# Optimization experiments

Hardware: AMD Instinct MI355X
Metric: run time of the kernel (lower is better)

## Reference

```python
import jax, jax.numpy as jnp
import numpy as np

B, NP, NC, E, C = 4, 512, 256, 128, 32
NBUCKET = 20


def soft_one_hot_linspace(x, start=0.0, end=15.0, number=NBUCKET):
    # e3nn soft_one_hot_linspace, basis='smooth_finite', cutoff=True
    values = jnp.linspace(start, end, number + 2)[1:-1]
    step = (end - start) / (number + 1)
    diff = (x[..., None] - values) / step

    def sus(y):  # exp(-1/y) for y>0 else 0 (smooth unit step)
        return jnp.where(y > 0.0, jnp.exp(-1.0 / jnp.where(y > 0.0, y, 1.0)), 0.0)

    return 1.14136 * jnp.exp(2.0) * sus(diff + 1.0) * sus(1.0 - diff)


def _init_linear(k, fan_in, fan_out):
    k1, k2 = jax.random.split(k)
    bound = 1.0 / np.sqrt(fan_in)
    W = jax.random.uniform(k1, (fan_in, fan_out), jnp.float32, -bound, bound)
    b = jax.random.uniform(k2, (fan_out,), jnp.float32, -bound, bound)
    return W, b


def setup_inputs() -> dict:
    key = jax.random.key(0)
    ks = jax.random.split(key, 12)
    inp = {}
    inp["z"] = jax.random.normal(ks[0], (B, NP, NC, E), jnp.float32)
    inp["z_mask"] = jax.random.randint(ks[1], (B, NP, NC), 0, 2) == 1
    inp["pocket_rep"] = jax.random.normal(ks[2], (B, NP, E), jnp.float32)
    inp["candidate_dis"] = jax.random.uniform(ks[3], (B, NP, NC), jnp.float32) * 16.0
    inp["W_lin"], inp["b_lin"] = _init_linear(ks[4], E, C)
    inp["W_dis"], inp["b_dis"] = _init_linear(ks[5], NBUCKET, C)
    inp["W_energy"], inp["b_energy"] = _init_linear(ks[6], C, 1)
    inp["W_gate"], inp["b_gate"] = _init_linear(ks[7], C, 1)
    inp["bias"] = jnp.ones((1,), jnp.float32)
    inp["W_energy_p"], inp["b_energy_p"] = _init_linear(ks[8], C, 1)
    inp["W_gate_p"], inp["b_gate_p"] = _init_linear(ks[9], C, 1)
    inp["bias_p"] = jnp.ones((1,), jnp.float32)
    inp["W_out"], inp["b_out"] = _init_linear(ks[10], E * C, E)
    return inp


def reference(z, z_mask, pocket_rep, candidate_dis,
              W_lin, b_lin, W_dis, b_dis,
              W_energy, b_energy, W_gate, b_gate, bias,
              W_energy_p, b_energy_p, W_gate_p, b_gate_p, bias_p,
              W_out, b_out):
    b, n_p, n_c, e = z.shape
    c = W_lin.shape[1]
    # linear + transpose(3,1): [B,Np,Nc,E] -> [B,C,Nc,Np]
    zc = jnp.transpose(z @ W_lin + b_lin, (0, 3, 2, 1))
    # softmax over last dim (Np)
    zc = jax.nn.softmax(zc, axis=-1)
    # distance-bucket bias: [B,Np,Nc,20] -> [B,Np,Nc,C] -> view [B,C,Nc,Np]
    edge_emb = soft_one_hot_linspace(candidate_dis)
    dis_bias = (edge_emb @ W_dis + b_dis).reshape(b, c, n_c, n_p)
    zc = zc + dis_bias
    # z_mask.repeat(C,1,1).view(B,C,Nc,Np) -- literal torch element order
    mask_rep = jnp.tile(z_mask, (c, 1, 1)).reshape(b, c, n_c, n_p)
    zc = jnp.where(mask_rep, jnp.asarray(1e-09, zc.dtype), zc)
    # gated energy heads on z.transpose(3,1): [B,Np,Nc,C]
    zt = jnp.transpose(zc, (0, 3, 2, 1))
    zm = z_mask.astype(zc.dtype)
    pair_energy = (jax.nn.sigmoid(zt @ W_gate + b_gate) * (zt @ W_energy + b_energy))[..., 0] * zm
    affinity_pred = jax.nn.leaky_relu(bias + pair_energy.sum(axis=(-1, -2)))
    pair_energy_p = (jax.nn.sigmoid(zt @ W_gate_p + b_gate_p) * (zt @ W_energy_p + b_energy_p))[..., 0] * zm
    prmsd_pred = jax.nn.leaky_relu(bias_p + pair_energy_p.sum(axis=(-1, -2)))
    # ligand rep: bmm([B,C*Nc,Np], [B,Np,E]) -> [B,Nc,C*E] -> Linear
    lig = jnp.einsum('bcln,bne->bcle', zc, pocket_rep)  # [B,C,Nc,E]
    lig = jnp.transpose(lig, (0, 2, 1, 3)).reshape(b, n_c, c * e)
    ligand_rep = lig @ W_out + b_out
    return (ligand_rep, affinity_pred, prmsd_pred)
```

## Files before the change

kernel.cpp:

```cpp
#include <hip/hip_runtime.h>
#include <stdint.h>


typedef float f32x4 __attribute__((ext_vector_type(4)));
typedef short s16x8 __attribute__((ext_vector_type(8)));

#define DEV static __device__ __forceinline__

DEV unsigned short f2bf(float f) {
  unsigned u = __builtin_bit_cast(unsigned, f);
  u += 0x7FFFu + ((u >> 16) & 1u);
  return (unsigned short)(u >> 16);
}
DEV float bf2f(unsigned short h) {
  unsigned u = ((unsigned)h) << 16;
  return __builtin_bit_cast(float, u);
}

__global__ void prep_k(const float* __restrict__ wlin,
                       const float* __restrict__ pocket,
                       const int* __restrict__ zmask,
                       const float* __restrict__ cdis,
                       unsigned short* __restrict__ wtlin,
                       unsigned short* __restrict__ pt,
                       unsigned long long* __restrict__ zmb,
                       unsigned long long* __restrict__ smb,
                       float* __restrict__ cdisT,
                       float* __restrict__ accg) {
  for (int i = blockIdx.x * 256 + threadIdx.x; i < 1839112; i += gridDim.x * 256) {
    if (i < 524288) {
      int np = i & 511, nc = (i >> 9) & 255, b = i >> 17;
      unsigned long long bal = __ballot(zmask[b * 131072 + np * 256 + nc] != 0);
      if ((i & 63) == 0) zmb[i >> 6] = bal;
    } else if (i < 1048576) {
      int o = i - 524288;
      int nn = o & 511, cm = (o >> 9) & 3, nc = o >> 11;
      unsigned long long bal = __ballot(zmask[cm * 131072 + nc * 512 + nn] != 0);
      if ((o & 63) == 0) smb[o >> 6] = bal;
    } else if (i < 1310720) {
      int o = i - 1048576;
      int np = o & 511, e = (o >> 9) & 127, b = o >> 16;
      pt[o] = f2bf(pocket[(b * 512 + np) * 128 + e]);
    } else if (i < 1314816) {
      int o = i - 1310720;
      int k = o & 127, c = o >> 7;
      wtlin[o] = f2bf(wlin[k * 32 + c]);
    } else if (i < 1314824) {
      accg[i - 1314816] = 0.0f;
    } else {
      int o = i - 1314824;
      int c = o & 31, np5 = (o >> 5) & 15, nc = (o >> 9) & 255, b = o >> 17;
      cdisT[o] = cdis[(b * 512 + 16 * c + (nc >> 4)) * 256 + 16 * (nc & 15) + np5];
    }
  }
}

__global__ void tr_k(const float* __restrict__ wout,
                     unsigned short* __restrict__ wto) {
  __shared__ float tile[64][65];
  const int kt = blockIdx.x, et = blockIdx.y;
  const int t = threadIdx.x;
  const int col = t & 63, r0 = t >> 6;
#pragma unroll
  for (int rr = 0; rr < 16; ++rr) {
    int row = rr * 4 + r0;
    tile[row][col] = wout[(kt * 64 + row) * 128 + et * 64 + col];
  }
  __syncthreads();
#pragma unroll
  for (int rr = 0; rr < 16; ++rr) {
    int erow = rr * 4 + r0;
    wto[(et * 64 + erow) * 4096 + kt * 64 + col] = f2bf(tile[col][erow]);
  }
}

extern __shared__ char smem[];

__global__ __launch_bounds__(256, 3) void mega_k(
    const float* __restrict__ z,
    const float* __restrict__ cdisT,
    const float* __restrict__ wdis, const float* __restrict__ bdis_g,
    const float* __restrict__ wE, const float* __restrict__ bE,
    const float* __restrict__ wG, const float* __restrict__ bG,
    const float* __restrict__ wEp, const float* __restrict__ bEp,
    const float* __restrict__ wGp, const float* __restrict__ bGp,
    const unsigned short* __restrict__ wtlin,
    const unsigned short* __restrict__ pt,
    const unsigned long long* __restrict__ zmb,
    const unsigned long long* __restrict__ smb,
    unsigned short* __restrict__ lig, float* __restrict__ accg) {
  const int nc = blockIdx.x, b = blockIdx.y;
  const int t = threadIdx.x;
  const int w = t >> 6, ln = t & 63;
  const int m16 = ln & 15, q = ln >> 4;

  unsigned short* T = (unsigned short*)smem;

  __shared__ float s_wd[640];
  __shared__ float s_bd[32];
  __shared__ float s_we[32], s_wg[32], s_wep[32], s_wgp[32];
  __shared__ float s_red[160];
  __shared__ float s_gmax[32], s_gsum[32];
  __shared__ unsigned long long s_mb[4][8];
  __shared__ unsigned long long s_zw[8];
  __shared__ float s_r8[8];

  if (t < 32) {
    s_bd[t] = bdis_g[t];
    s_we[t] = wE[t]; s_wg[t] = wG[t];
    s_wep[t] = wEp[t]; s_wgp[t] = wGp[t];
    s_mb[t >> 3][t & 7] = smb[nc * 32 + t];
  }
  if (t >= 32 && t < 40) s_zw[t - 32] = zmb[(b * 256 + nc) * 8 + (t - 32)];
  for (int i = t; i < 640; i += 256) s_wd[i] = wdis[i];

  f32x4 acc1[8][2];
#pragma unroll
  for (int i = 0; i < 8; ++i) {
    acc1[i][0] = f32x4{0.f, 0.f, 0.f, 0.f};
    acc1[i][1] = f32x4{0.f, 0.f, 0.f, 0.f};
  }
  const float* zb = z + (size_t)b * 16777216 + (size_t)nc * 128;
  for (int k0 = 0; k0 < 128; k0 += 32) {
    s16x8 bf0 = *(const s16x8*)(wtlin + m16 * 128 + k0 + q * 8);
    s16x8 bf1 = *(const s16x8*)(wtlin + (16 + m16) * 128 + k0 + q * 8);
#pragma unroll
    for (int bt = 0; bt < 4; ++bt) {
      f32x4 z0[2], z1[2];
#pragma unroll
      for (int i = 0; i < 2; ++i) {
        int np = (w * 8 + bt * 2 + i) * 16 + m16;
        const float* p = zb + (size_t)np * 32768 + k0 + q * 8;
        z0[i] = *(const f32x4*)p;
        z1[i] = *(const f32x4*)(p + 4);
      }
#pragma unroll
      for (int i = 0; i < 2; ++i) {
        s16x8 af;
        af[0] = (short)f2bf(z0[i][0]); af[1] = (short)f2bf(z0[i][1]);
        af[2] = (short)f2bf(z0[i][2]); af[3] = (short)f2bf(z0[i][3]);
        af[4] = (short)f2bf(z1[i][0]); af[5] = (short)f2bf(z1[i][1]);
        af[6] = (short)f2bf(z1[i][2]); af[7] = (short)f2bf(z1[i][3]);
        int ai = bt * 2 + i;
        acc1[ai][0] = __builtin_amdgcn_mfma_f32_16x16x32_bf16(af, bf0, acc1[ai][0], 0, 0, 0);
        acc1[ai][1] = __builtin_amdgcn_mfma_f32_16x16x32_bf16(af, bf1, acc1[ai][1], 0, 0, 0);
      }
    }
  }

  float mx[2] = {-3.0e38f, -3.0e38f};
#pragma unroll
  for (int ai = 0; ai < 8; ++ai)
#pragma unroll
    for (int ct = 0; ct < 2; ++ct)
#pragma unroll
      for (int r = 0; r < 4; ++r) mx[ct] = fmaxf(mx[ct], acc1[ai][ct][r]);
#pragma unroll
  for (int ct = 0; ct < 2; ++ct) {
    float v = mx[ct];
    v = fmaxf(v, __shfl_xor(v, 16));
    v = fmaxf(v, __shfl_xor(v, 32));
    mx[ct] = v;
  }
  if (ln < 16) { s_red[ln * 5 + w] = mx[0]; s_red[(16 + ln) * 5 + w] = mx[1]; }
  __syncthreads();
  if (t < 32)
    s_gmax[t] = fmaxf(fmaxf(s_red[t * 5], s_red[t * 5 + 1]),
                      fmaxf(s_red[t * 5 + 2], s_red[t * 5 + 3]));
  __syncthreads();
  float sm[2] = {0.f, 0.f};
#pragma unroll
  for (int ct = 0; ct < 2; ++ct) {
    float g = s_gmax[ct * 16 + m16];
#pragma unroll
    for (int ai = 0; ai < 8; ++ai)
#pragma unroll
      for (int r = 0; r < 4; ++r) {
        float e = __expf(acc1[ai][ct][r] - g);
        acc1[ai][ct][r] = e;
        sm[ct] += e;
      }
  }
#pragma unroll
  for (int ct = 0; ct < 2; ++ct) {
    float v = sm[ct];
    v += __shfl_xor(v, 16);
    v += __shfl_xor(v, 32);
    sm[ct] = v;
  }
  if (ln < 16) { s_red[ln * 5 + w] = sm[0]; s_red[(16 + ln) * 5 + w] = sm[1]; }
  __syncthreads();
  if (t < 32)
    s_gsum[t] = 1.0f / (s_red[t * 5] + s_red[t * 5 + 1] + s_red[t * 5 + 2] + s_red[t * 5 + 3]);
  __syncthreads();

#pragma unroll
  for (int ct = 0; ct < 2; ++ct) {
    int c = ct * 16 + m16;
    float s = s_gsum[c];
#pragma unroll
    for (int ai = 0; ai < 8; ++ai) {
      int npb = (w * 8 + ai) * 16 + q * 4;
      unsigned lo = (unsigned)f2bf(acc1[ai][ct][0] * s) |
                    ((unsigned)f2bf(acc1[ai][ct][1] * s) << 16);
      unsigned hi = (unsigned)f2bf(acc1[ai][ct][2] * s) |
                    ((unsigned)f2bf(acc1[ai][ct][3] * s) << 16);
      *(uint2*)(T + c * 520 + npb) = make_uint2(lo, hi);
    }
  }
  __syncthreads();

  {
    const float SUSK = 8.4335794f;
    const float* cdb = cdisT + (size_t)(b * 256 + nc) * 512;
#pragma unroll
    for (int tt = 0; tt < 2; ++tt) {
      int task = t + tt * 256;
      int c = task & 31, np5 = task >> 5;
      float d = cdb[task];
      float val[32];
#pragma unroll
      for (int kk = 0; kk < 32; ++kk) val[kk] = s_bd[kk];
      for (int j = 0; j < 20; ++j) {
        float diff = d * (21.0f / 15.0f) - (float)(j + 1);
        float y1 = diff + 1.f, y2 = 1.f - diff;
        float u = 0.f;
        if (y1 > 0.f && y2 > 0.f) u = SUSK * __expf(-1.f / y1 - 1.f / y2);
#pragma unroll
        for (int kk = 0; kk < 32; ++kk) val[kk] += u * s_wd[j * 32 + kk];
      }
      int npb = np5 * 32;
      unsigned long long mw = s_mb[c & 3][npb >> 6];
#pragma unroll
      for (int kb2 = 0; kb2 < 4; ++kb2) {
        unsigned short* tp = T + c * 520 + npb + kb2 * 8;
        s16x8 tv = *(s16x8*)tp;
        s16x8 ov;
#pragma unroll
        for (int kk = 0; kk < 8; ++kk) {
          float x = bf2f((unsigned short)tv[kk]) + val[kb2 * 8 + kk];
          int mk = (int)((mw >> ((npb + kb2 * 8 + kk) & 63)) & 1ull);
          ov[kk] = (short)f2bf(mk ? 1e-9f : x);
        }
        *(s16x8*)tp = ov;
      }
    }
  }
  __syncthreads();

  {
    float aff = 0.f, prm = 0.f;
    const float bg0 = bG[0], be0 = bE[0], bgp0 = bGp[0], bep0 = bEp[0];
#pragma unroll
    for (int s = 0; s < 2; ++s) {
      int np = s * 256 + t;
      float g = bg0, e = be0, gp = bgp0, ep = bep0;
      for (int c = 0; c < 32; ++c) {
        float tv = bf2f(T[c * 520 + np]);
        g += tv * s_wg[c]; e += tv * s_we[c];
        gp += tv * s_wgp[c]; ep += tv * s_wep[c];
      }
      if ((s_zw[np >> 6] >> (np & 63)) & 1ull) {
        aff += e / (1.f + __expf(-g));
        prm += ep / (1.f + __expf(-gp));
      }
    }
#pragma unroll
    for (int d = 32; d >= 1; d >>= 1) {
      aff += __shfl_xor(aff, d);
      prm += __shfl_xor(prm, d);
    }
    if (ln == 0) { s_r8[w] = aff; s_r8[4 + w] = prm; }
    __syncthreads();
    if (t == 0) {
      atomicAdd(accg + b, s_r8[0] + s_r8[1] + s_r8[2] + s_r8[3]);
      atomicAdd(accg + 4 + b, s_r8[4] + s_r8[5] + s_r8[6] + s_r8[7]);
    }
  }

  {
    f32x4 a5[2][2];
    a5[0][0] = f32x4{0.f, 0.f, 0.f, 0.f}; a5[0][1] = a5[0][0];
    a5[1][0] = a5[0][0]; a5[1][1] = a5[0][0];
    const unsigned short* ptb = pt + b * 65536;
    for (int k0 = 0; k0 < 512; k0 += 32) {
      s16x8 aT0 = *(const s16x8*)(T + m16 * 520 + k0 + q * 8);
      s16x8 aT1 = *(const s16x8*)(T + (16 + m16) * 520 + k0 + q * 8);
      s16x8 bP0 = *(const s16x8*)(ptb + (w * 32 + m16) * 512 + k0 + q * 8);
      s16x8 bP1 = *(const s16x8*)(ptb + (w * 32 + 16 + m16) * 512 + k0 + q * 8);
      a5[0][0] = __builtin_amdgcn_mfma_f32_16x16x32_bf16(aT0, bP0, a5[0][0], 0, 0, 0);
      a5[0][1] = __builtin_amdgcn_mfma_f32_16x16x32_bf16(aT0, bP1, a5[0][1], 0, 0, 0);
      a5[1][0] = __builtin_amdgcn_mfma_f32_16x16x32_bf16(aT1, bP0, a5[1][0], 0, 0, 0);
      a5[1][1] = __builtin_amdgcn_mfma_f32_16x16x32_bf16(aT1, bP1, a5[1][1], 0, 0, 0);
    }
    unsigned short* lg = lig + (size_t)(b * 256 + nc) * 4096;
#pragma unroll
    for (int mt = 0; mt < 2; ++mt)
#pragma unroll
      for (int u = 0; u < 2; ++u)
#pragma unroll
        for (int r = 0; r < 4; ++r) {
          int c = mt * 16 + q * 4 + r;
          int e = w * 32 + u * 16 + m16;
          lg[c * 128 + e] = f2bf(a5[mt][u][r]);
        }
  }
}

__global__ __launch_bounds__(256, 2) void proj_k(
    const unsigned short* __restrict__ lig, const unsigned short* __restrict__ wto,
    float* __restrict__ part) {
  const int mb = blockIdx.x, ks = blockIdx.y;
  const int t = threadIdx.x, w = t >> 6, ln = t & 63;
  const int m16 = ln & 15, q = ln >> 4;
  f32x4 acc[8];
#pragma unroll
  for (int nt = 0; nt < 8; ++nt) acc[nt] = f32x4{0.f, 0.f, 0.f, 0.f};
  const int kb = ks * 512;
  const int row = mb * 64 + w * 16 + m16;
  for (int k0 = 0; k0 < 512; k0 += 32) {
    s16x8 af = *(const s16x8*)(lig + (size_t)row * 4096 + kb + k0 + q * 8);
    s16x8 bf[8];
#pragma unroll
    for (int nt = 0; nt < 8; ++nt)
      bf[nt] = *(const s16x8*)(wto + (size_t)(nt * 16 + m16) * 4096 + kb + k0 + q * 8);
#pragma unroll
    for (int nt = 0; nt < 8; ++nt)
      acc[nt] = __builtin_amdgcn_mfma_f32_16x16x32_bf16(af, bf[nt], acc[nt], 0, 0, 0);
  }
  float* pp = part + (size_t)ks * 131072 + (size_t)(mb * 64 + w * 16) * 128;
#pragma unroll
  for (int nt = 0; nt < 8; ++nt)
#pragma unroll
    for (int r = 0; r < 4; ++r)
      pp[(q * 4 + r) * 128 + nt * 16 + m16] = acc[nt][r];
}

__global__ void reduce_k(const float* __restrict__ part, const float* __restrict__ bout,
                         const float* __restrict__ accg, const float* __restrict__ bias,
                         const float* __restrict__ biasp, float* __restrict__ outp) {
  int i = blockIdx.x * 256 + threadIdx.x;
  float s = bout[i & 127];
#pragma unroll
  for (int ks = 0; ks < 8; ++ks) s += part[(size_t)ks * 131072 + i];
  outp[i] = s;
  if (blockIdx.x == 0 && threadIdx.x < 8) {
    int tt = threadIdx.x;
    float base = (tt < 4) ? bias[0] : biasp[0];
    float x = base + accg[tt];
    outp[131072 + tt] = (x >= 0.f) ? x : 0.01f * x;
  }
}

extern "C" void kernel_launch(void* const* d_in, const int* in_sizes, int n_in,
                              void* d_out, int out_size, void* d_ws, size_t ws_size,
                              hipStream_t stream) {
  const float* z      = (const float*)d_in[0];
  const int*   zmask  = (const int*)d_in[1];
  const float* pocket = (const float*)d_in[2];
  const float* cdis   = (const float*)d_in[3];
  const float* wlin   = (const float*)d_in[4];
  const float* wdis   = (const float*)d_in[6];
  const float* bdis   = (const float*)d_in[7];
  const float* wE     = (const float*)d_in[8];
  const float* bE     = (const float*)d_in[9];
  const float* wG     = (const float*)d_in[10];
  const float* bG     = (const float*)d_in[11];
  const float* bias   = (const float*)d_in[12];
  const float* wEp    = (const float*)d_in[13];
  const float* bEp    = (const float*)d_in[14];
  const float* wGp    = (const float*)d_in[15];
  const float* bGp    = (const float*)d_in[16];
  const float* biasp  = (const float*)d_in[17];
  const float* wout   = (const float*)d_in[18];
  const float* bout   = (const float*)d_in[19];

  char* ws = (char*)d_ws;
  float* accg                  = (float*)(ws + 0);
  unsigned short* wtlin        = (unsigned short*)(ws + 1024);
  unsigned long long* zmb      = (unsigned long long*)(ws + 16384);
  unsigned long long* smb      = (unsigned long long*)(ws + 81920);
  unsigned short* pt           = (unsigned short*)(ws + 393216);
  float* cdisT                 = (float*)(ws + 1048576);
  unsigned short* wto          = (unsigned short*)(ws + 3145728);
  unsigned short* lig          = (unsigned short*)(ws + 4194304);
  float* part                  = (float*)(ws + 12582912);
  float* outp = (float*)d_out;

  prep_k<<<1024, 256, 0, stream>>>(wlin, pocket, zmask, cdis,
                                   wtlin, pt, zmb, smb, cdisT, accg);
  tr_k<<<dim3(64, 2), 256, 0, stream>>>(wout, wto);
  mega_k<<<dim3(256, 4), 256, 33280, stream>>>(z, cdisT, wdis, bdis,
      wE, bE, wG, bG, wEp, bEp, wGp, bGp, wtlin, pt, zmb, smb, lig, accg);
  proj_k<<<dim3(16, 8), 256, 0, stream>>>(lig, wto, part);
  reduce_k<<<512, 256, 0, stream>>>(part, bout, accg, bias, biasp, outp);
}
```

Measured before the change: 486.2 us.

## Split z projection and softmax into separate kernel using LDS DMA loads

Moves the z·W_lin MFMA projection and the softmax over Np out of the mega kernel into a new kernel. The new kernel stages z rows into LDS with global_load_lds DMA in chunks of 64 rows, then writes the bf16 softmax tile to a global workspace. The remaining mega kernel reads that tile back into shared memory, and both kernels now request occupancy 4. The aim is to get more coalesced, higher-occupancy streaming of the large z tensor, at the cost of an extra launch and a global round trip of the softmax tile (about 32 MB of bf16).

Result: slower. 496.7 us (+2.2%).

```diff
diff --git a/kernel.cpp b/kernel.cpp
--- a/kernel.cpp
+++ b/kernel.cpp
@@ -15,6 +15,12 @@
 DEV float bf2f(unsigned short h) {
   unsigned u = ((unsigned)h) << 16;
   return __builtin_bit_cast(float, u);
+}
+
+DEV void dma16(const float* g, const float* l) {
+  __builtin_amdgcn_global_load_lds(
+      (const __attribute__((address_space(1))) unsigned*)g,
+      (__attribute__((address_space(3))) unsigned*)l, 16, 0, 0);
 }
 
 __global__ void prep_k(const float* __restrict__ wlin,
@@ -74,17 +80,131 @@
   }
 }
 
+__global__ __launch_bounds__(256, 4) void zsm_k(
+    const float* __restrict__ z,
+    const unsigned short* __restrict__ wtlin,
+    unsigned short* __restrict__ Tg) {
+  const int nc = blockIdx.x, b = blockIdx.y;
+  const int t = threadIdx.x;
+  const int w = t >> 6, ln = t & 63;
+  const int m16 = ln & 15, q = ln >> 4;
+
+  __shared__ float buf[8192];
+  __shared__ float s_red[160];
+  __shared__ float s_gmax[32], s_gsum[32];
+
+  const float* zb = z + (size_t)b * 16777216 + (size_t)nc * 128;
+  const float* ldst = buf + w * 2048;
+  const int lrow_off = (ln >> 5);
+  const int lcol = (ln & 31) * 4;
+
+  f32x4 acc1[8][2];
+#pragma unroll
+  for (int i = 0; i < 8; ++i) {
+    acc1[i][0] = f32x4{0.f, 0.f, 0.f, 0.f};
+    acc1[i][1] = f32x4{0.f, 0.f, 0.f, 0.f};
+  }
+
+#pragma unroll
+  for (int ch = 0; ch < 8; ++ch) {
+#pragma unroll
+    for (int i = 0; i < 8; ++i) {
+      int row = ch * 64 + w * 16 + i * 2 + lrow_off;
+      dma16(zb + (size_t)row * 32768 + lcol, ldst + i * 256);
+    }
+    __syncthreads();
+#pragma unroll
+    for (int k0i = 0; k0i < 4; ++k0i) {
+      const int k0 = k0i * 32;
+      s16x8 bf0 = *(const s16x8*)(wtlin + m16 * 128 + k0 + q * 8);
+      s16x8 bf1 = *(const s16x8*)(wtlin + (16 + m16) * 128 + k0 + q * 8);
+      const float* rowp = buf + (w * 16 + m16) * 128 + k0 + q * 8;
+      f32x4 z0 = *(const f32x4*)rowp;
+      f32x4 z1 = *(const f32x4*)(rowp + 4);
+      s16x8 af;
+      af[0] = (short)f2bf(z0[0]); af[1] = (short)f2bf(z0[1]);
+      af[2] = (short)f2bf(z0[2]); af[3] = (short)f2bf(z0[3]);
+      af[4] = (short)f2bf(z1[0]); af[5] = (short)f2bf(z1[1]);
+      af[6] = (short)f2bf(z1[2]); af[7] = (short)f2bf(z1[3]);
+      acc1[ch][0] = __builtin_amdgcn_mfma_f32_16x16x32_bf16(af, bf0, acc1[ch][0], 0, 0, 0);
+      acc1[ch][1] = __builtin_amdgcn_mfma_f32_16x16x32_bf16(af, bf1, acc1[ch][1], 0, 0, 0);
+    }
+    __syncthreads();
+  }
+
+  float mx[2] = {-3.0e38f, -3.0e38f};
+#pragma unroll
+  for (int ch = 0; ch < 8; ++ch)
+#pragma unroll
+    for (int ct = 0; ct < 2; ++ct)
+#pragma unroll
+      for (int r = 0; r < 4; ++r) mx[ct] = fmaxf(mx[ct], acc1[ch][ct][r]);
+#pragma unroll
+  for (int ct = 0; ct < 2; ++ct) {
+    float v = mx[ct];
+    v = fmaxf(v, __shfl_xor(v, 16));
+    v = fmaxf(v, __shfl_xor(v, 32));
+    mx[ct] = v;
+  }
+  if (ln < 16) { s_red[ln * 5 + w] = mx[0]; s_red[(16 + ln) * 5 + w] = mx[1]; }
+  __syncthreads();
+  if (t < 32)
+    s_gmax[t] = fmaxf(fmaxf(s_red[t * 5], s_red[t * 5 + 1]),
+                      fmaxf(s_red[t * 5 + 2], s_red[t * 5 + 3]));
+  __syncthreads();
+  float sm[2] = {0.f, 0.f};
+#pragma unroll
+  for (int ct = 0; ct < 2; ++ct) {
+    float g = s_gmax[ct * 16 + m16];
+#pragma unroll
+    for (int ch = 0; ch < 8; ++ch)
+#pragma unroll
+      for (int r = 0; r < 4; ++r) {
+        float e = __expf(acc1[ch][ct][r] - g);
+        acc1[ch][ct][r] = e;
+        sm[ct] += e;
+      }
+  }
+#pragma unroll
+  for (int ct = 0; ct < 2; ++ct) {
+    float v = sm[ct];
+    v += __shfl_xor(v, 16);
+    v += __shfl_xor(v, 32);
+    sm[ct] = v;
+  }
+  if (ln < 16) { s_red[ln * 5 + w] = sm[0]; s_red[(16 + ln) * 5 + w] = sm[1]; }
+  __syncthreads();
+  if (t < 32)
+    s_gsum[t] = 1.0f / (s_red[t * 5] + s_red[t * 5 + 1] + s_red[t * 5 + 2] + s_red[t * 5 + 3]);
+  __syncthreads();
+
+  unsigned short* tg = Tg + (size_t)(b * 256 + nc) * 16384;
+#pragma unroll
+  for (int ct = 0; ct < 2; ++ct) {
+    int c = ct * 16 + m16;
+    float s = s_gsum[c];
+#pragma unroll
+    for (int ch = 0; ch < 8; ++ch) {
+      int npb = ch * 64 + w * 16 + q * 4;
+      unsigned lo = (unsigned)f2bf(acc1[ch][ct][0] * s) |
+                    ((unsigned)f2bf(acc1[ch][ct][1] * s) << 16);
+      unsigned hi = (unsigned)f2bf(acc1[ch][ct][2] * s) |
+                    ((unsigned)f2bf(acc1[ch][ct][3] * s) << 16);
+      *(uint2*)(tg + c * 512 + npb) = make_uint2(lo, hi);
+    }
+  }
+}
+
 extern __shared__ char smem[];
 
-__global__ __launch_bounds__(256, 3) void mega_k(
-    const float* __restrict__ z,
+__global__ __launch_bounds__(256, 4) void mega2_k(
+    const unsigned short* __restrict__ Tg,
     const float* __restrict__ cdisT,
     const float* __restrict__ wdis, const float* __restrict__ bdis_g,
     const float* __restrict__ wE, const float* __restrict__ bE,
     const float* __restrict__ wG, const float* __restrict__ bG,
     const float* __restrict__ wEp, const float* __restrict__ bEp,
     const float* __restrict__ wGp, const float* __restrict__ bGp,
-    const unsigned short* __restrict__ wtlin,
     const unsigned short* __restrict__ pt,
     const unsigned long long* __restrict__ zmb,
     const unsigned long long* __restrict__ smb,
@@ -99,8 +219,6 @@
   __shared__ float s_wd[640];
   __shared__ float s_bd[32];
   __shared__ float s_we[32], s_wg[32], s_wep[32], s_wgp[32];
-  __shared__ float s_red[160];
-  __shared__ float s_gmax[32], s_gsum[32];
   __shared__ unsigned long long s_mb[4][8];
   __shared__ unsigned long long s_zw[8];
   __shared__ float s_r8[8];
@@ -114,99 +232,12 @@
   if (t >= 32 && t < 40) s_zw[t - 32] = zmb[(b * 256 + nc) * 8 + (t - 32)];
   for (int i = t; i < 640; i += 256) s_wd[i] = wdis[i];
 
-  f32x4 acc1[8][2];
-#pragma unroll
-  for (int i = 0; i < 8; ++i) {
-    acc1[i][0] = f32x4{0.f, 0.f, 0.f, 0.f};
-    acc1[i][1] = f32x4{0.f, 0.f, 0.f, 0.f};
-  }
-  const float* zb = z + (size_t)b * 16777216 + (size_t)nc * 128;
-  for (int k0 = 0; k0 < 128; k0 += 32) {
-    s16x8 bf0 = *(const s16x8*)(wtlin + m16 * 128 + k0 + q * 8);
-    s16x8 bf1 = *(const s16x8*)(wtlin + (16 + m16) * 128 + k0 + q * 8);
-#pragma unroll
-    for (int bt = 0; bt < 4; ++bt) {
-      f32x4 z0[2], z1[2];
-#pragma unroll
-      for (int i = 0; i < 2; ++i) {
-        int np = (w * 8 + bt * 2 + i) * 16 + m16;
-        const float* p = zb + (size_t)np * 32768 + k0 + q * 8;
-        z0[i] = *(const f32x4*)p;
-        z1[i] = *(const f32x4*)(p + 4);
-      }
-#pragma unroll
-      for (int i = 0; i < 2; ++i) {
-        s16x8 af;
-        af[0] = (short)f2bf(z0[i][0]); af[1] = (short)f2bf(z0[i][1]);
-        af[2] = (short)f2bf(z0[i][2]); af[3] = (short)f2bf(z0[i][3]);
-        af[4] = (short)f2bf(z1[i][0]); af[5] = (short)f2bf(z1[i][1]);
-        af[6] = (short)f2bf(z1[i][2]); af[7] = (short)f2bf(z1[i][3]);
-        int ai = bt * 2 + i;
-        acc1[ai][0] = __builtin_amdgcn_mfma_f32_16x16x32_bf16(af, bf0, acc1[ai][0], 0, 0, 0);
-        acc1[ai][1] = __builtin_amdgcn_mfma_f32_16x16x32_bf16(af, bf1, acc1[ai][1], 0, 0, 0);
-      }
-    }
-  }
-
-  float mx[2] = {-3.0e38f, -3.0e38f};
-#pragma unroll
-  for (int ai = 0; ai < 8; ++ai)
-#pragma unroll
-    for (int ct = 0; ct < 2; ++ct)
-#pragma unroll
-      for (int r = 0; r < 4; ++r) mx[ct] = fmaxf(mx[ct], acc1[ai][ct][r]);
-#pragma unroll
-  for (int ct = 0; ct < 2; ++ct) {
-    float v = mx[ct];
-    v = fmaxf(v, __shfl_xor(v, 16));
-    v = fmaxf(v, __shfl_xor(v, 32));
-    mx[ct] = v;
-  }
-  if (ln < 16) { s_red[ln * 5 + w] = mx[0]; s_red[(16 + ln) * 5 + w] = mx[1]; }
-  __syncthreads();
-  if (t < 32)
-    s_gmax[t] = fmaxf(fmaxf(s_red[t * 5], s_red[t * 5 + 1]),
-                      fmaxf(s_red[t * 5 + 2], s_red[t * 5 + 3]));
-  __syncthreads();
-  float sm[2] = {0.f, 0.f};
-#pragma unroll
-  for (int ct = 0; ct < 2; ++ct) {
-    float g = s_gmax[ct * 16 + m16];
-#pragma unroll
-    for (int ai = 0; ai < 8; ++ai)
-#pragma unroll
-      for (int r = 0; r < 4; ++r) {
-        float e = __expf(acc1[ai][ct][r] - g);
-        acc1[ai][ct][r] = e;
-        sm[ct] += e;
-      }
-  }
-#pragma unroll
-  for (int ct = 0; ct < 2; ++ct) {
-    float v = sm[ct];
-    v += __shfl_xor(v, 16);
-    v += __shfl_xor(v, 32);
-    sm[ct] = v;
-  }
-  if (ln < 16) { s_red[ln * 5 + w] = sm[0]; s_red[(16 + ln) * 5 + w] = sm[1]; }
-  __syncthreads();
-  if (t < 32)
-    s_gsum[t] = 1.0f / (s_red[t * 5] + s_red[t * 5 + 1] + s_red[t * 5 + 2] + s_red[t * 5 + 3]);
-  __syncthreads();
-
-#pragma unroll
-  for (int ct = 0; ct < 2; ++ct) {
-    int c = ct * 16 + m16;
-    float s = s_gsum[c];
-#pragma unroll
-    for (int ai = 0; ai < 8; ++ai) {
-      int npb = (w * 8 + ai) * 16 + q * 4;
-      unsigned lo = (unsigned)f2bf(acc1[ai][ct][0] * s) |
-                    ((unsigned)f2bf(acc1[ai][ct][1] * s) << 16);
-      unsigned hi = (unsigned)f2bf(acc1[ai][ct][2] * s) |
-                    ((unsigned)f2bf(acc1[ai][ct][3] * s) << 16);
-      *(uint2*)(T + c * 520 + npb) = make_uint2(lo, hi);
-    }
+  const unsigned short* tg = Tg + (size_t)(b * 256 + nc) * 16384;
+#pragma unroll
+  for (int j = 0; j < 8; ++j) {
+    int f = j * 256 + t;
+    int c = f >> 6, off = (f & 63) * 8;
+    *(s16x8*)(T + c * 520 + off) = *(const s16x8*)(tg + f * 8);
   }
   __syncthreads();
 
@@ -385,13 +416,15 @@
   unsigned short* wto          = (unsigned short*)(ws + 3145728);
   unsigned short* lig          = (unsigned short*)(ws + 4194304);
   float* part                  = (float*)(ws + 12582912);
+  unsigned short* Tg           = (unsigned short*)(ws + 16777216);
   float* outp = (float*)d_out;
 
   prep_k<<<1024, 256, 0, stream>>>(wlin, pocket, zmask, cdis,
                                    wtlin, pt, zmb, smb, cdisT, accg);
   tr_k<<<dim3(64, 2), 256, 0, stream>>>(wout, wto);
-  mega_k<<<dim3(256, 4), 256, 33280, stream>>>(z, cdisT, wdis, bdis,
-      wE, bE, wG, bG, wEp, bEp, wGp, bGp, wtlin, pt, zmb, smb, lig, accg);
+  zsm_k<<<dim3(256, 4), 256, 0, stream>>>(z, wtlin, Tg);
+  mega2_k<<<dim3(256, 4), 256, 33280, stream>>>(Tg, cdisT, wdis, bdis,
+      wE, bE, wG, bG, wEp, bEp, wGp, bGp, pt, zmb, smb, lig, accg);
   proj_k<<<dim3(16, 8), 256, 0, stream>>>(lig, wto, part);
   reduce_k<<<512, 256, 0, stream>>>(part, bout, accg, bias, biasp, outp);
 }
```
